# Kernel optimization log

Hardware: AMD Instinct MI355X
Metric: run time of the kernel (lower is better)

The kernel has to match this reference:

```python
import jax, jax.numpy as jnp
import numpy as np

DIM = 768
NUM_HEADS = 12
HEAD_DIM = DIM // NUM_HEADS
SCALE = HEAD_DIM ** -0.5
B, N = 16, 640  # N = 8*8 + 24*24


def setup_inputs() -> dict:
    key = jax.random.key(0)
    ks = jax.random.split(key, 4)
    x = jax.random.normal(ks[0], (B, N, DIM), dtype=jnp.float32)
    # weights stored input-major: y = x @ W + b (equiv. to torch Linear with W = weight.T)
    qkv_w = jax.random.normal(ks[1], (DIM, 3 * DIM), dtype=jnp.float32) * (DIM ** -0.5)
    qkv_b = jnp.zeros((3 * DIM,), dtype=jnp.float32)
    proj_w = jax.random.normal(ks[2], (DIM, DIM), dtype=jnp.float32) * (DIM ** -0.5)
    proj_b = jnp.zeros((DIM,), dtype=jnp.float32)
    w = jnp.ones((2,), dtype=jnp.float32)
    return {"x": x, "qkv_w": qkv_w, "qkv_b": qkv_b, "proj_w": proj_w,
            "proj_b": proj_b, "w": w, "t_h": 8, "t_w": 8, "s_h": 24, "s_w": 24}


def reference(x, qkv_w, qkv_b, proj_w, proj_b, w, t_h, t_w, s_h, s_w):
    b, n, c = x.shape
    qkv = (x @ qkv_w + qkv_b).reshape(b, n, 3, NUM_HEADS, HEAD_DIM)
    qkv = jnp.transpose(qkv, (2, 0, 3, 1, 4))  # [3, B, H, N, D]
    q, k, v = qkv[0], qkv[1], qkv[2]
    attn = jnp.einsum('bhnd,bhmd->bhnm', q, k) * SCALE  # [B,H,N,N]
    attn0 = jax.nn.softmax(attn, axis=-1)
    attn1 = jnp.square(jax.nn.relu(attn))
    ws = jax.nn.softmax(w)  # exp(w_i)/sum(exp(w)) blend weights
    attn = attn0 * ws[0] + attn1 * ws[1]
    out = jnp.einsum('bhnm,bhmd->bhnd', attn, v)  # [B,H,N,D]
    out = jnp.transpose(out, (0, 2, 1, 3)).reshape(b, n, c)
    return out @ proj_w + proj_b
```

## Files before the change

### kernel.cpp

```cpp
#include <hip/hip_runtime.h>
#include <hip/hip_bf16.h>

typedef __attribute__((ext_vector_type(8))) short short8;
typedef __attribute__((ext_vector_type(4))) float floatx4;
typedef __hip_bfloat16 bf16;

#define DIM 768
#define NH 12
#define HD 64
#define BB 16
#define NN 640
#define BH (BB*NH)
#define MROWS (BB*NN)
#define QKVN (3*DIM)
#define QSCALE 0.18033688011113205f
#define LN2SQ 0.4804530139182014f

#define CVT_BLK (MROWS*DIM/4/256)
#define TRQ_BLK ((QKVN/32)*(DIM/32))
#define TRP_BLK ((DIM/32)*(DIM/32))

__device__ __forceinline__ floatx4 mfma16(short8 a, short8 b, floatx4 c) {
    return __builtin_amdgcn_mfma_f32_16x16x32_bf16(a, b, c, 0, 0, 0);
}

__device__ __forceinline__ void async_ld16(const bf16* g, bf16* l) {
    __builtin_amdgcn_global_load_lds(
        (const __attribute__((address_space(1))) void*)g,
        (__attribute__((address_space(3))) void*)l, 16, 0, 0);
}

__device__ __forceinline__ unsigned pack_trunc(float a, float b) {
    return __builtin_amdgcn_perm(__float_as_uint(b), __float_as_uint(a), 0x07060302u);
}

__device__ __forceinline__ unsigned pack_rne(float a, float b) {
    unsigned sa = (unsigned)__bfloat16_as_ushort(__float2bfloat16(a));
    unsigned sb = (unsigned)__bfloat16_as_ushort(__float2bfloat16(b));
    return sa | (sb << 16);
}

__device__ __forceinline__ float fexp2(float x) {
#if __has_builtin(__builtin_amdgcn_exp2f)
    return __builtin_amdgcn_exp2f(x);
#else
    return exp2f(x);
#endif
}

__global__ void prep_all(const float* __restrict__ x,
                         const float* __restrict__ qkv_w,
                         const float* __restrict__ proj_w,
                         bf16* __restrict__ xb,
                         bf16* __restrict__ qwT,
                         bf16* __restrict__ pwT)
{
    __shared__ float tile[32][33];
    const int id = blockIdx.x;
    const int t = threadIdx.x;

    if (id < CVT_BLK) {
        int i = id * 256 + t;
        float4 v = ((const float4*)x)[i];
        *(uint2*)(xb + (size_t)i * 4) =
            make_uint2(pack_rne(v.x, v.y), pack_rne(v.z, v.w));
        return;
    }

    const float* src; bf16* dst; int C, bx, by;
    if (id < CVT_BLK + TRQ_BLK) {
        int j = id - CVT_BLK;
        bx = j % (QKVN/32); by = j / (QKVN/32);
        src = qkv_w; dst = qwT; C = QKVN;
    } else {
        int j = id - CVT_BLK - TRQ_BLK;
        bx = j % (DIM/32); by = j / (DIM/32);
        src = proj_w; dst = pwT; C = DIM;
    }
    const int R = DIM;
    const int tx = t & 31, ty = t >> 5;
    for (int j = 0; j < 4; ++j)
        tile[ty + j*8][tx] = src[(size_t)(by*32 + ty + j*8) * C + bx*32 + tx];
    __syncthreads();
    for (int j = 0; j < 4; ++j)
        dst[(size_t)(bx*32 + ty + j*8) * R + by*32 + tx] = __float2bfloat16(tile[tx][ty + j*8]);
}

template<int MODE>
__global__ __launch_bounds__(256) void gemm_bt(
    const bf16* __restrict__ A, const bf16* __restrict__ B, const float* __restrict__ bias,
    int M, int N, int K,
    bf16* __restrict__ outb, bf16* __restrict__ vTo, float* __restrict__ outf)
{
    __shared__ __align__(16) bf16 As[2][128*64];
    __shared__ __align__(16) bf16 Bs[2][128*64];

    const int t = threadIdx.x;
    const int lane = t & 63, wave = t >> 6;
    const int l15 = lane & 15, quad = lane >> 4;
    const int wm = (wave >> 1) * 64, wn = (wave & 1) * 64;

    constexpr int GX  = (MODE == 0) ? (QKVN/128) : (DIM/128);
    constexpr int NWG = GX * (MROWS/128);
    constexpr int CHUNK = NWG / 8;
    int lin = blockIdx.y * GX + blockIdx.x;
    lin = (lin & 7) * CHUNK + (lin >> 3);
    const int m0 = (lin / GX) * 128, n0 = (lin % GX) * 128;

    floatx4 acc[4][4];
    floatx4 zero = {0.f, 0.f, 0.f, 0.f};
    for (int i = 0; i < 4; ++i)
        for (int j = 0; j < 4; ++j)
            acc[i][j] = zero;

    const int trow = t >> 3;
    const int gc = ((t & 7) ^ (trow & 7)) << 3;
    const bf16* aA = A + (size_t)(m0 + trow) * K + gc;
    const bf16* aB = B + (size_t)(n0 + trow) * K + gc;
    const int lb = wave * 512;

    for (int s = 0; s < 4; ++s) {
        async_ld16(aA + (size_t)s*32*K, &As[0][s*2048 + lb]);
        async_ld16(aB + (size_t)s*32*K, &Bs[0][s*2048 + lb]);
    }

    const int sw = l15 & 7;
    const int nit = K >> 6;
    for (int kt = 0; kt < nit; ++kt) {
        const int cur = kt & 1;
        __syncthreads();
        if (kt + 1 < nit) {
            const bf16* pA = aA + (size_t)(kt+1)*64;
            const bf16* pB = aB + (size_t)(kt+1)*64;
            for (int s = 0; s < 4; ++s) {
                async_ld16(pA + (size_t)s*32*K, &As[cur^1][s*2048 + lb]);
                async_ld16(pB + (size_t)s*32*K, &Bs[cur^1][s*2048 + lb]);
            }
        }
        short8 af0[4], af1[4], bf0[4], bf1[4];
        for (int fm = 0; fm < 4; ++fm) {
            int base = (wm + fm*16 + l15) * 64 + ((quad ^ sw) << 3);
            af0[fm] = *(const short8*)(&As[cur][base]);
            af1[fm] = *(const short8*)(&As[cur][base ^ 32]);
        }
        for (int fn = 0; fn < 4; ++fn) {
            int base = (wn + fn*16 + l15) * 64 + ((quad ^ sw) << 3);
            bf0[fn] = *(const short8*)(&Bs[cur][base]);
            bf1[fn] = *(const short8*)(&Bs[cur][base ^ 32]);
        }
        for (int fm = 0; fm < 4; ++fm)
            for (int fn = 0; fn < 4; ++fn) {
                acc[fm][fn] = mfma16(bf0[fn], af0[fm], acc[fm][fn]);
                acc[fm][fn] = mfma16(bf1[fn], af1[fm], acc[fm][fn]);
            }
    }

    if (MODE == 0 && n0 >= 2*DIM) {
        bf16* S = &As[0][0] + wave * 2048;
        unsigned short* Su = (unsigned short*)S;
        const int bh   = (m0 / NN) * NH + ((n0 + wn) >> 6) - 24;
        const int tokb = (m0 % NN) + wm;
        const int dl = lane >> 2, cc = (lane & 3) * 16;
        for (int fn = 0; fn < 4; ++fn) {
            int nb = n0 + wn + fn*16 + quad*4;
            float4 bv = *(const float4*)(bias + nb);
            float bvr[4] = {bv.x, bv.y, bv.z, bv.w};
            for (int fm = 0; fm < 4; ++fm) {
#pragma unroll
                for (int r = 0; r < 4; ++r) {
                    float v = acc[fm][fn][r] + bvr[r];
                    Su[(quad*4 + r)*72 + fm*16 + l15] =
                        (unsigned short)(__float_as_uint(v) >> 16);
                }
            }
            uint4 r0 = *(const uint4*)(S + dl*72 + cc);
            uint4 r1 = *(const uint4*)(S + dl*72 + cc + 8);
            bf16* dst = vTo + ((size_t)bh * HD + fn*16 + dl) * NN + tokb + cc;
            *(uint4*)dst = r0;
            *(uint4*)(dst + 8) = r1;
        }
        return;
    }

    for (int fm = 0; fm < 4; ++fm) {
        int m = m0 + wm + fm*16 + l15;
        if (MODE == 0) {
            bf16* row = outb + (size_t)m * N;
            for (int fn = 0; fn < 4; ++fn) {
                int n = n0 + wn + fn*16 + quad*4;
                float4 bv = *(const float4*)(bias + n);
                float v0 = acc[fm][fn][0] + bv.x;
                float v1 = acc[fm][fn][1] + bv.y;
                float v2 = acc[fm][fn][2] + bv.z;
                float v3 = acc[fm][fn][3] + bv.w;
                if (n < DIM) {
                    v0 *= QSCALE; v1 *= QSCALE; v2 *= QSCALE; v3 *= QSCALE;
                }
                *(uint2*)(row + n) = make_uint2(pack_rne(v0, v1), pack_rne(v2, v3));
            }
        } else {
            float* row = outf + (size_t)m * N;
            for (int fn = 0; fn < 4; ++fn) {
                int n = n0 + wn + fn*16 + quad*4;
                float4 bv = *(const float4*)(bias + n);
                float4 v;
                v.x = acc[fm][fn][0] + bv.x;
                v.y = acc[fm][fn][1] + bv.y;
                v.z = acc[fm][fn][2] + bv.z;
                v.w = acc[fm][fn][3] + bv.w;
                *(float4*)(row + n) = v;
            }
        }
    }
}

__global__ __launch_bounds__(256) void attn_kernel(
    const bf16* __restrict__ qkv, const bf16* __restrict__ vT,
    const float* __restrict__ w2, bf16* __restrict__ ao)
{
    int lin = blockIdx.y * BH + blockIdx.x;
    int j = lin >> 3;
    const int bh = (lin & 7) + 8 * (j / 10);
    const int qt = j % 10;
    const int b = bh / NH, h = bh - b * NH;
    const int t = threadIdx.x;
    const int wave = t >> 6, lane = t & 63;
    const int l15 = lane & 15, quad = lane >> 4;
    const int qrow0 = qt * 64 + wave * 16;

    float w0 = w2[0], w1 = w2[1];
    float wmx = fmaxf(w0, w1);
    float e0 = __expf(w0 - wmx), e1 = __expf(w1 - wmx);
    float ws0 = e0 / (e0 + e1);
    float ws1 = (1.0f - ws0) * LN2SQ;

    __shared__ __align__(16) bf16 Kb[2][64*64];
    __shared__ __align__(16) bf16 Vb[2][64*64];
    __shared__ __align__(16) bf16 Ps[4][16*72];
    __shared__ __align__(16) bf16 Pr[4][16*72];

    const bf16* kb = qkv + (size_t)(b*NN)*QKVN + DIM + h*HD;
    const bf16* vb = vT + (size_t)bh * HD * NN;

    const bf16* qr = qkv + (size_t)(b*NN + qrow0 + l15) * QKVN + h*HD;
    short8 aq0 = *(const short8*)(qr + quad*8);
    short8 aq1 = *(const short8*)(qr + 32 + quad*8);

    const int srow = t >> 3;
    const int gc   = ((lane & 7) ^ (lane >> 3)) << 3;
    const bf16* kst = kb + (size_t)srow * QKVN + gc;
    const bf16* vst = vb + (size_t)srow * NN + gc;
    const int lb0 = (wave * 64) * 8;
    const int lb1 = (256 + wave * 64) * 8;

    async_ld16(kst,                     &Kb[0][lb0]);
    async_ld16(kst + (size_t)32 * QKVN, &Kb[0][lb1]);
    async_ld16(vst,                     &Vb[0][lb0]);
    async_ld16(vst + (size_t)32 * NN,   &Vb[0][lb1]);

    floatx4 zero = {0.f, 0.f, 0.f, 0.f};
    floatx4 accS[4], accR[4];
    for (int i = 0; i < 4; ++i) { accS[i] = zero; accR[i] = zero; }
    float lsum = 0.f;

    const int sw = l15 & 7;
    const int fbase = l15 * 64 + ((quad ^ sw) << 3);

    unsigned* PsW = (unsigned*)&Ps[wave][0];
    unsigned* PrW = (unsigned*)&Pr[wave][0];
    const int wb = l15*36 + quad*2;
    const bf16* PsR = &Ps[wave][l15*72 + quad*8];
    const bf16* PrR = &Pr[wave][l15*72 + quad*8];

#pragma unroll 2
    for (int kt = 0; kt < 10; ++kt) {
        const int cur = kt & 1;
        __syncthreads();
        if (kt + 1 < 10) {
            kst += (size_t)64 * QKVN;
            vst += 64;
            async_ld16(kst,                     &Kb[cur^1][lb0]);
            async_ld16(kst + (size_t)32 * QKVN, &Kb[cur^1][lb1]);
            async_ld16(vst,                     &Vb[cur^1][lb0]);
            async_ld16(vst + (size_t)32 * NN,   &Vb[cur^1][lb1]);
        }

        const bf16* Kc = &Kb[cur][0];
        const bf16* Vc = &Vb[cur][0];

        floatx4 s[4];
        for (int I = 0; I < 4; ++I) {
            short8 aklo = *(const short8*)(Kc + fbase + I*1024);
            short8 akhi = *(const short8*)(Kc + ((fbase + I*1024) ^ 32));
            s[I] = zero;
            s[I] = mfma16(aklo, aq0, s[I]);
            s[I] = mfma16(akhi, aq1, s[I]);
        }

        short8 bvlo[4], bvhi[4];
        for (int dt = 0; dt < 4; ++dt) {
            bvlo[dt] = *(const short8*)(Vc + fbase + dt*1024);
            bvhi[dt] = *(const short8*)(Vc + ((fbase + dt*1024) ^ 32));
        }

        for (int I = 0; I < 4; ++I) {
            float ex[4], rq[4];
            for (int r = 0; r < 4; ++r) {
                ex[r] = fexp2(s[I][r]);
                float m = fmaxf(s[I][r], 0.f);
                rq[r] = m * m;
                lsum += ex[r];
            }
            *(uint2*)(PsW + wb + I*8) = make_uint2(pack_trunc(ex[0],ex[1]), pack_trunc(ex[2],ex[3]));
            *(uint2*)(PrW + wb + I*8) = make_uint2(pack_trunc(rq[0],rq[1]), pack_trunc(rq[2],rq[3]));
        }

        short8 paSlo = *(const short8*)PsR;
        short8 paShi = *(const short8*)(PsR + 32);
        short8 paRlo = *(const short8*)PrR;
        short8 paRhi = *(const short8*)(PrR + 32);

        for (int dt = 0; dt < 4; ++dt) {
            accS[dt] = mfma16(paSlo, bvlo[dt], accS[dt]);
            accS[dt] = mfma16(paShi, bvhi[dt], accS[dt]);
            accR[dt] = mfma16(paRlo, bvlo[dt], accR[dt]);
            accR[dt] = mfma16(paRhi, bvhi[dt], accR[dt]);
        }
    }

    lsum += __shfl_xor(lsum, 16);
    lsum += __shfl_xor(lsum, 32);
    float invq[4];
    for (int r = 0; r < 4; ++r)
        invq[r] = 1.0f / __shfl(lsum, quad*4 + r);

    for (int dt = 0; dt < 4; ++dt) {
        for (int r = 0; r < 4; ++r) {
            float v = ws0 * accS[dt][r] * invq[r] + ws1 * accR[dt][r];
            int tok = qrow0 + quad*4 + r;
            ao[((size_t)(b * NN + tok)) * DIM + h * HD + dt*16 + l15] = __float2bfloat16(v);
        }
    }
}


extern "C" void kernel_launch(void* const* d_in, const int* in_sizes, int n_in,
                              void* d_out, int out_size, void* d_ws, size_t ws_size,
                              hipStream_t stream) {
    const float* x      = (const float*)d_in[0];
    const float* qkv_w  = (const float*)d_in[1];
    const float* qkv_b  = (const float*)d_in[2];
    const float* proj_w = (const float*)d_in[3];
    const float* proj_b = (const float*)d_in[4];
    const float* w2     = (const float*)d_in[5];
    float* out = (float*)d_out;

    bf16* xb   = (bf16*)d_ws;
    bf16* qwT  = xb   + (size_t)MROWS * DIM;
    bf16* pwT  = qwT  + (size_t)QKVN * DIM;
    bf16* qkvb = pwT  + (size_t)DIM * DIM;
    bf16* vT   = qkvb + (size_t)MROWS * QKVN;
    bf16* ao   = xb;

    prep_all<<<CVT_BLK + TRQ_BLK + TRP_BLK, 256, 0, stream>>>(
        x, qkv_w, proj_w, xb, qwT, pwT);

    gemm_bt<0><<<dim3(QKVN / 128, MROWS / 128), 256, 0, stream>>>(
        xb, qwT, qkv_b, MROWS, QKVN, DIM, qkvb, vT, nullptr);

    attn_kernel<<<dim3(BH, NN / 64), 256, 0, stream>>>(qkvb, vT, w2, ao);

    gemm_bt<1><<<dim3(DIM / 128, MROWS / 128), 256, 0, stream>>>(
        ao, pwT, proj_b, MROWS, DIM, DIM, nullptr, nullptr, out);
}
```

Before: 217.7 us.

## Add 256x256-tile 8-wave QKV GEMM with phased async staging

Replaces the 128x128 QKV projection GEMM with a dedicated kernel that uses 256x256 output tiles, 512 threads, and a four-phase-per-buffer schedule. Global-to-LDS async loads are interleaved with MFMA phases, using setprio and explicit waitcnt/barriers. The aim is to raise arithmetic intensity and hide load latency. It uses 128KB of LDS per block, and the grid becomes 9x40 = 360 blocks, which may leave CUs unevenly loaded. The V-transpose epilogue is reworked for the new wave layout.

Result: slower. 227.4 us (+4.4%).

```diff
diff --git a/kernel.cpp b/kernel.cpp
--- a/kernel.cpp
+++ b/kernel.cpp
@@ -84,6 +84,179 @@
     __syncthreads();
     for (int j = 0; j < 4; ++j)
         dst[(size_t)(bx*32 + ty + j*8) * R + by*32 + tx] = __float2bfloat16(tile[tx][ty + j*8]);
+}
+
+__global__ __launch_bounds__(512, 2) void gemm_qkv256(
+    const bf16* __restrict__ A, const bf16* __restrict__ B, const float* __restrict__ bias,
+    bf16* __restrict__ outb, bf16* __restrict__ vTo)
+{
+    constexpr int K = DIM;
+    constexpr int N = QKVN;
+    __shared__ __align__(16) bf16 As[2][2][128*64];
+    __shared__ __align__(16) bf16 Bs[2][2][128*64];
+
+    const int t = threadIdx.x;
+    const int lane = t & 63, wave = t >> 6;
+    const int l15 = lane & 15, quad = lane >> 4;
+    const int wm = wave >> 2;
+    const int wn = wave & 3;
+    const int hB = wn >> 1;
+    const int m0 = blockIdx.y * 256, n0 = blockIdx.x * 256;
+
+    floatx4 acc[8][4];
+    floatx4 zero = {0.f, 0.f, 0.f, 0.f};
+#pragma unroll
+    for (int i = 0; i < 8; ++i)
+#pragma unroll
+        for (int j = 0; j < 4; ++j)
+            acc[i][j] = zero;
+
+    const int trow = t >> 3;
+    const int gc = ((t & 7) ^ (trow & 7)) << 3;
+    const bf16* Ag = A + (size_t)(m0 + trow) * K + gc;
+    const bf16* Bg = B + (size_t)(n0 + trow) * K + gc;
+    const int tb = t * 8;
+
+#define STG_A(buf,h,s,tcol) async_ld16(Ag + (size_t)((h)*128+(s)*64)*K + (tcol), &As[buf][h][(s)*4096 + tb])
+#define STG_B(buf,h,s,tcol) async_ld16(Bg + (size_t)((h)*128+(s)*64)*K + (tcol), &Bs[buf][h][(s)*4096 + tb])
+
+    const int swq = (quad ^ (l15 & 7)) << 3;
+    const int aoff = l15 * 64 + swq;
+    const int boff = (wn & 1) * 4096 + l15 * 64 + swq;
+
+    short8 bfr[4][2];
+
+#define RD_B(buf) do { \
+    _Pragma("unroll") \
+    for (int fn = 0; fn < 4; ++fn) { \
+        const int _ob = boff + fn*1024; \
+        bfr[fn][0] = *(const short8*)&Bs[buf][hB][_ob]; \
+        bfr[fn][1] = *(const short8*)&Bs[buf][hB][_ob ^ 32]; \
+    } } while (0)
+
+#define PHASE(buf, q, RB, STAGES, WAITS) do { \
+    const int _o = aoff + (2*(q))*1024; \
+    short8 a00 = *(const short8*)&As[buf][wm][_o]; \
+    short8 a01 = *(const short8*)&As[buf][wm][_o ^ 32]; \
+    short8 a10 = *(const short8*)&As[buf][wm][_o + 1024]; \
+    short8 a11 = *(const short8*)&As[buf][wm][(_o + 1024) ^ 32]; \
+    RB; \
+    STAGES; \
+    __builtin_amdgcn_s_barrier(); \
+    asm volatile("s_waitcnt lgkmcnt(0)" ::: "memory"); \
+    __builtin_amdgcn_sched_barrier(0); \
+    __builtin_amdgcn_s_setprio(1); \
+    _Pragma("unroll") \
+    for (int fn = 0; fn < 4; ++fn) { \
+        acc[2*(q)][fn]   = mfma16(bfr[fn][0], a00, acc[2*(q)][fn]); \
+        acc[2*(q)+1][fn] = mfma16(bfr[fn][0], a10, acc[2*(q)+1][fn]); \
+    } \
+    _Pragma("unroll") \
+    for (int fn = 0; fn < 4; ++fn) { \
+        acc[2*(q)][fn]   = mfma16(bfr[fn][1], a01, acc[2*(q)][fn]); \
+        acc[2*(q)+1][fn] = mfma16(bfr[fn][1], a11, acc[2*(q)+1][fn]); \
+    } \
+    __builtin_amdgcn_s_setprio(0); \
+    WAITS; \
+    __builtin_amdgcn_s_barrier(); \
+} while (0)
+
+    STG_B(0,0,0,0); STG_B(0,0,1,0); STG_B(0,1,0,0); STG_B(0,1,1,0);
+    STG_A(0,0,0,0); STG_A(0,1,0,0); STG_A(0,0,1,0); STG_A(0,1,1,0);
+    STG_B(1,0,0,64); STG_B(1,0,1,64); STG_B(1,1,0,64); STG_B(1,1,1,64);
+    STG_A(1,0,0,64); STG_A(1,1,0,64);
+    asm volatile("s_waitcnt vmcnt(6)" ::: "memory");
+    __builtin_amdgcn_s_barrier();
+
+    for (int it = 0; it < 6; ++it) {
+        const int kb = it * 128;
+        const bool more = (it < 5);
+        PHASE(0, 0, RD_B(0),
+              { STG_A(1,0,1,kb+64); STG_A(1,1,1,kb+64); },
+              (void)0);
+        PHASE(0, 1, (void)0,
+              { if (more) { STG_B(0,0,0,kb+128); STG_B(0,0,1,kb+128); } },
+              (void)0);
+        PHASE(0, 2, (void)0,
+              { if (more) { STG_B(0,1,0,kb+128); STG_B(0,1,1,kb+128); } },
+              (void)0);
+        PHASE(0, 3, (void)0,
+              { if (more) { STG_A(0,0,0,kb+128); STG_A(0,1,0,kb+128); } },
+              { if (more) { asm volatile("s_waitcnt vmcnt(6)" ::: "memory"); }
+                else      { asm volatile("s_waitcnt vmcnt(0)" ::: "memory"); } });
+        PHASE(1, 0, RD_B(1),
+              { if (more) { STG_A(0,0,1,kb+128); STG_A(0,1,1,kb+128); } },
+              (void)0);
+        PHASE(1, 1, (void)0,
+              { if (more) { STG_B(1,0,0,kb+192); STG_B(1,0,1,kb+192); } },
+              (void)0);
+        PHASE(1, 2, (void)0,
+              { if (more) { STG_B(1,1,0,kb+192); STG_B(1,1,1,kb+192); } },
+              (void)0);
+        PHASE(1, 3, (void)0,
+              { if (more) { STG_A(1,0,0,kb+192); STG_A(1,1,0,kb+192); } },
+              { if (more) { asm volatile("s_waitcnt vmcnt(6)" ::: "memory"); } });
+    }
+#undef PHASE
+#undef RD_B
+#undef STG_A
+#undef STG_B
+
+    const int mb = m0 + wm * 128;
+    const int nb = n0 + wn * 64;
+
+    if (n0 >= 2*DIM) {
+        bf16* S = &As[0][0][0] + wave * 2048;
+        unsigned short* Su = (unsigned short*)S;
+        const int head = (nb - 2*DIM) >> 6;
+        const int gm = mb;
+        const int bh = (gm / NN) * NH + head;
+        const int tokb = gm % NN;
+        const int dl = lane >> 2, cc = (lane & 3) * 16;
+#pragma unroll
+        for (int fmh = 0; fmh < 2; ++fmh) {
+#pragma unroll
+            for (int fn = 0; fn < 4; ++fn) {
+                int nq = nb + fn*16 + quad*4;
+                float4 bv = *(const float4*)(bias + nq);
+                float bvr[4] = {bv.x, bv.y, bv.z, bv.w};
+#pragma unroll
+                for (int fi = 0; fi < 4; ++fi) {
+#pragma unroll
+                    for (int r = 0; r < 4; ++r) {
+                        float v = acc[fmh*4 + fi][fn][r] + bvr[r];
+                        Su[(quad*4 + r)*72 + fi*16 + l15] =
+                            (unsigned short)(__float_as_uint(v) >> 16);
+                    }
+                }
+                uint4 r0 = *(const uint4*)(S + dl*72 + cc);
+                uint4 r1 = *(const uint4*)(S + dl*72 + cc + 8);
+                int d = fn*16 + dl;
+                bf16* dst = vTo + ((size_t)bh * HD + d) * NN + tokb + fmh*64 + cc;
+                *(uint4*)dst = r0;
+                *(uint4*)(dst + 8) = r1;
+            }
+        }
+        return;
+    }
+
+    const bool isq = (n0 < DIM);
+#pragma unroll
+    for (int fm = 0; fm < 8; ++fm) {
+        int m = mb + fm*16 + l15;
+        bf16* row = outb + (size_t)m * N;
+#pragma unroll
+        for (int fn = 0; fn < 4; ++fn) {
+            int n = nb + fn*16 + quad*4;
+            float4 bv = *(const float4*)(bias + n);
+            float v0 = acc[fm][fn][0] + bv.x;
+            float v1 = acc[fm][fn][1] + bv.y;
+            float v2 = acc[fm][fn][2] + bv.z;
+            float v3 = acc[fm][fn][3] + bv.w;
+            if (isq) { v0 *= QSCALE; v1 *= QSCALE; v2 *= QSCALE; v3 *= QSCALE; }
+            *(uint2*)(row + n) = make_uint2(pack_rne(v0, v1), pack_rne(v2, v3));
+        }
+    }
 }
 
 template<int MODE>
@@ -365,8 +538,8 @@
     prep_all<<<CVT_BLK + TRQ_BLK + TRP_BLK, 256, 0, stream>>>(
         x, qkv_w, proj_w, xb, qwT, pwT);
 
-    gemm_bt<0><<<dim3(QKVN / 128, MROWS / 128), 256, 0, stream>>>(
-        xb, qwT, qkv_b, MROWS, QKVN, DIM, qkvb, vT, nullptr);
+    gemm_qkv256<<<dim3(QKVN / 256, MROWS / 256), 512, 0, stream>>>(
+        xb, qwT, qkv_b, qkvb, vT);
 
     attn_kernel<<<dim3(BH, NN / 64), 256, 0, stream>>>(qkvb, vT, w2, ao);
 
```

## Use 256x128 tiles with 8 waves and ping-pong scheduled GEMM pipeline

Applied to the files above, without the earlier changes.

Replaces the 128x128, 4-wave GEMM with a 256x128-tile, 8-wave kernel with compile-time shapes. The K loop is software-pipelined: each step stages two 64-wide K slices, explicit vmcnt/lgkmcnt waits and barriers interleave global loads with MFMA halves, and s_setprio raises priority during MFMA. The aim is better tile reuse and overlap of memory traffic with matrix math in both the QKV and output-projection GEMMs. In exchange it relies on hand-tuned wait counts and uses more shared memory, and the larger tiles give fewer workgroups.

Result: slower. 225.3 us (+3.5%).

```diff
diff --git a/kernel.cpp b/kernel.cpp
--- a/kernel.cpp
+++ b/kernel.cpp
@@ -87,84 +87,133 @@
 }
 
 template<int MODE>
-__global__ __launch_bounds__(256) void gemm_bt(
+__global__ __launch_bounds__(512, 2) void gemm256(
     const bf16* __restrict__ A, const bf16* __restrict__ B, const float* __restrict__ bias,
-    int M, int N, int K,
     bf16* __restrict__ outb, bf16* __restrict__ vTo, float* __restrict__ outf)
 {
-    __shared__ __align__(16) bf16 As[2][128*64];
+    constexpr int K = DIM;
+    constexpr int N = (MODE == 0) ? QKVN : DIM;
+    constexpr int GX = N / 128;
+    constexpr int NWG = GX * (MROWS / 256);
+    constexpr int CHUNK = NWG / 8;
+
+    __shared__ __align__(16) bf16 As[2][256*64];
     __shared__ __align__(16) bf16 Bs[2][128*64];
 
     const int t = threadIdx.x;
     const int lane = t & 63, wave = t >> 6;
     const int l15 = lane & 15, quad = lane >> 4;
-    const int wm = (wave >> 1) * 64, wn = (wave & 1) * 64;
-
-    constexpr int GX  = (MODE == 0) ? (QKVN/128) : (DIM/128);
-    constexpr int NWG = GX * (MROWS/128);
-    constexpr int CHUNK = NWG / 8;
-    int lin = blockIdx.y * GX + blockIdx.x;
+    const int wm = wave >> 1;
+    const int wn = wave & 1;
+
+    int lin = blockIdx.x;
     lin = (lin & 7) * CHUNK + (lin >> 3);
-    const int m0 = (lin / GX) * 128, n0 = (lin % GX) * 128;
+    const int m0 = (lin / GX) * 256, n0 = (lin % GX) * 128;
 
     floatx4 acc[4][4];
     floatx4 zero = {0.f, 0.f, 0.f, 0.f};
+#pragma unroll
     for (int i = 0; i < 4; ++i)
+#pragma unroll
         for (int j = 0; j < 4; ++j)
             acc[i][j] = zero;
 
     const int trow = t >> 3;
     const int gc = ((t & 7) ^ (trow & 7)) << 3;
-    const bf16* aA = A + (size_t)(m0 + trow) * K + gc;
-    const bf16* aB = B + (size_t)(n0 + trow) * K + gc;
-    const int lb = wave * 512;
-
-    for (int s = 0; s < 4; ++s) {
-        async_ld16(aA + (size_t)s*32*K, &As[0][s*2048 + lb]);
-        async_ld16(aB + (size_t)s*32*K, &Bs[0][s*2048 + lb]);
-    }
-
-    const int sw = l15 & 7;
-    const int nit = K >> 6;
-    for (int kt = 0; kt < nit; ++kt) {
-        const int cur = kt & 1;
-        __syncthreads();
-        if (kt + 1 < nit) {
-            const bf16* pA = aA + (size_t)(kt+1)*64;
-            const bf16* pB = aB + (size_t)(kt+1)*64;
-            for (int s = 0; s < 4; ++s) {
-                async_ld16(pA + (size_t)s*32*K, &As[cur^1][s*2048 + lb]);
-                async_ld16(pB + (size_t)s*32*K, &Bs[cur^1][s*2048 + lb]);
-            }
-        }
-        short8 af0[4], af1[4], bf0[4], bf1[4];
-        for (int fm = 0; fm < 4; ++fm) {
-            int base = (wm + fm*16 + l15) * 64 + ((quad ^ sw) << 3);
-            af0[fm] = *(const short8*)(&As[cur][base]);
-            af1[fm] = *(const short8*)(&As[cur][base ^ 32]);
-        }
-        for (int fn = 0; fn < 4; ++fn) {
-            int base = (wn + fn*16 + l15) * 64 + ((quad ^ sw) << 3);
-            bf0[fn] = *(const short8*)(&Bs[cur][base]);
-            bf1[fn] = *(const short8*)(&Bs[cur][base ^ 32]);
-        }
-        for (int fm = 0; fm < 4; ++fm)
-            for (int fn = 0; fn < 4; ++fn) {
-                acc[fm][fn] = mfma16(bf0[fn], af0[fm], acc[fm][fn]);
-                acc[fm][fn] = mfma16(bf1[fn], af1[fm], acc[fm][fn]);
-            }
-    }
+    const bf16* Ag = A + (size_t)(m0 + trow) * K + gc;
+    const bf16* Bg = B + (size_t)(n0 + trow) * K + gc;
+    const int tb = t * 8;
+
+#define STG_A(buf,s,tcol) async_ld16(Ag + (size_t)(s)*64*K + (tcol), &As[buf][(s)*4096 + tb])
+#define STG_B(buf,s,tcol) async_ld16(Bg + (size_t)(s)*64*K + (tcol), &Bs[buf][(s)*4096 + tb])
+
+    const int sw8 = (quad ^ (l15 & 7)) << 3;
+    const int aoff = (wm*64 + l15) * 64 + sw8;
+    const int boff = (wn*64 + l15) * 64 + sw8;
+
+    short8 afr[4][2], bfr[4][2];
+
+#define RD_FRAGS(buf) do { \
+    _Pragma("unroll") \
+    for (int f = 0; f < 4; ++f) { \
+        afr[f][0] = *(const short8*)&As[buf][aoff + f*1024]; \
+        afr[f][1] = *(const short8*)&As[buf][(aoff + f*1024) ^ 32]; \
+        bfr[f][0] = *(const short8*)&Bs[buf][boff + f*1024]; \
+        bfr[f][1] = *(const short8*)&Bs[buf][(boff + f*1024) ^ 32]; \
+    } } while (0)
+
+#define MFMA_HALF(q) do { \
+    __builtin_amdgcn_s_setprio(1); \
+    _Pragma("unroll") \
+    for (int fn = 0; fn < 4; ++fn) { \
+        acc[2*(q)][fn]   = mfma16(bfr[fn][0], afr[2*(q)][0],   acc[2*(q)][fn]); \
+        acc[2*(q)+1][fn] = mfma16(bfr[fn][0], afr[2*(q)+1][0], acc[2*(q)+1][fn]); \
+    } \
+    _Pragma("unroll") \
+    for (int fn = 0; fn < 4; ++fn) { \
+        acc[2*(q)][fn]   = mfma16(bfr[fn][1], afr[2*(q)][1],   acc[2*(q)][fn]); \
+        acc[2*(q)+1][fn] = mfma16(bfr[fn][1], afr[2*(q)+1][1], acc[2*(q)+1][fn]); \
+    } \
+    __builtin_amdgcn_s_setprio(0); \
+} while (0)
+
+    STG_A(0,0,0); STG_A(0,1,0); STG_A(0,2,0); STG_A(0,3,0);
+    STG_B(0,0,0); STG_B(0,1,0);
+    STG_A(1,0,64); STG_A(1,1,64); STG_A(1,2,64); STG_A(1,3,64);
+    STG_B(1,0,64); STG_B(1,1,64);
+    asm volatile("s_waitcnt vmcnt(6)" ::: "memory");
+    __builtin_amdgcn_s_barrier();
+
+    for (int it = 0; it < 6; ++it) {
+        const int kb = it * 128;
+        const bool more = (it < 5);
+        RD_FRAGS(0);
+        __builtin_amdgcn_s_barrier();
+        asm volatile("s_waitcnt lgkmcnt(0)" ::: "memory");
+        __builtin_amdgcn_sched_barrier(0);
+        MFMA_HALF(0);
+        __builtin_amdgcn_s_barrier();
+        if (more) { STG_A(0,0,kb+128); STG_A(0,1,kb+128); STG_A(0,2,kb+128); STG_A(0,3,kb+128); }
+        MFMA_HALF(1);
+        __builtin_amdgcn_sched_barrier(0);
+        if (more) { asm volatile("s_waitcnt vmcnt(4)" ::: "memory"); }
+        else      { asm volatile("s_waitcnt vmcnt(0)" ::: "memory"); }
+        __builtin_amdgcn_s_barrier();
+        RD_FRAGS(1);
+        if (more) { STG_B(0,0,kb+128); STG_B(0,1,kb+128); }
+        __builtin_amdgcn_s_barrier();
+        asm volatile("s_waitcnt lgkmcnt(0)" ::: "memory");
+        __builtin_amdgcn_sched_barrier(0);
+        MFMA_HALF(0);
+        __builtin_amdgcn_s_barrier();
+        if (more) { STG_A(1,0,kb+192); STG_A(1,1,kb+192); STG_A(1,2,kb+192); STG_A(1,3,kb+192);
+                    STG_B(1,0,kb+192); STG_B(1,1,kb+192); }
+        MFMA_HALF(1);
+        __builtin_amdgcn_sched_barrier(0);
+        if (more) { asm volatile("s_waitcnt vmcnt(6)" ::: "memory"); }
+        __builtin_amdgcn_s_barrier();
+    }
+#undef RD_FRAGS
+#undef MFMA_HALF
+#undef STG_A
+#undef STG_B
+
+    const int mb = m0 + wm * 64;
+    const int nb = n0 + wn * 64;
 
     if (MODE == 0 && n0 >= 2*DIM) {
         bf16* S = &As[0][0] + wave * 2048;
         unsigned short* Su = (unsigned short*)S;
-        const int bh   = (m0 / NN) * NH + ((n0 + wn) >> 6) - 24;
-        const int tokb = (m0 % NN) + wm;
+        const int head = ((nb - 2*DIM) >> 6);
+        const int bh = (mb / NN) * NH + head;
+        const int tokb = mb % NN;
         const int dl = lane >> 2, cc = (lane & 3) * 16;
+#pragma unroll
         for (int fn = 0; fn < 4; ++fn) {
-            int nb = n0 + wn + fn*16 + quad*4;
-            float4 bv = *(const float4*)(bias + nb);
+            int nq = nb + fn*16 + quad*4;
+            float4 bv = *(const float4*)(bias + nq);
             float bvr[4] = {bv.x, bv.y, bv.z, bv.w};
+#pragma unroll
             for (int fm = 0; fm < 4; ++fm) {
 #pragma unroll
                 for (int r = 0; r < 4; ++r) {
@@ -175,33 +224,40 @@
             }
             uint4 r0 = *(const uint4*)(S + dl*72 + cc);
             uint4 r1 = *(const uint4*)(S + dl*72 + cc + 8);
-            bf16* dst = vTo + ((size_t)bh * HD + fn*16 + dl) * NN + tokb + cc;
+            int d = fn*16 + dl;
+            bf16* dst = vTo + ((size_t)bh * HD + d) * NN + tokb + cc;
             *(uint4*)dst = r0;
             *(uint4*)(dst + 8) = r1;
         }
         return;
     }
 
-    for (int fm = 0; fm < 4; ++fm) {
-        int m = m0 + wm + fm*16 + l15;
-        if (MODE == 0) {
+    if (MODE == 0) {
+        const bool isq = (n0 < DIM);
+#pragma unroll
+        for (int fm = 0; fm < 4; ++fm) {
+            int m = mb + fm*16 + l15;
             bf16* row = outb + (size_t)m * N;
+#pragma unroll
             for (int fn = 0; fn < 4; ++fn) {
-                int n = n0 + wn + fn*16 + quad*4;
+                int n = nb + fn*16 + quad*4;
                 float4 bv = *(const float4*)(bias + n);
                 float v0 = acc[fm][fn][0] + bv.x;
                 float v1 = acc[fm][fn][1] + bv.y;
                 float v2 = acc[fm][fn][2] + bv.z;
                 float v3 = acc[fm][fn][3] + bv.w;
-                if (n < DIM) {
-                    v0 *= QSCALE; v1 *= QSCALE; v2 *= QSCALE; v3 *= QSCALE;
-                }
+                if (isq) { v0 *= QSCALE; v1 *= QSCALE; v2 *= QSCALE; v3 *= QSCALE; }
                 *(uint2*)(row + n) = make_uint2(pack_rne(v0, v1), pack_rne(v2, v3));
             }
-        } else {
+        }
+    } else {
+#pragma unroll
+        for (int fm = 0; fm < 4; ++fm) {
+            int m = mb + fm*16 + l15;
             float* row = outf + (size_t)m * N;
+#pragma unroll
             for (int fn = 0; fn < 4; ++fn) {
-                int n = n0 + wn + fn*16 + quad*4;
+                int n = nb + fn*16 + quad*4;
                 float4 bv = *(const float4*)(bias + n);
                 float4 v;
                 v.x = acc[fm][fn][0] + bv.x;
@@ -365,11 +421,11 @@
     prep_all<<<CVT_BLK + TRQ_BLK + TRP_BLK, 256, 0, stream>>>(
         x, qkv_w, proj_w, xb, qwT, pwT);
 
-    gemm_bt<0><<<dim3(QKVN / 128, MROWS / 128), 256, 0, stream>>>(
-        xb, qwT, qkv_b, MROWS, QKVN, DIM, qkvb, vT, nullptr);
+    gemm256<0><<<dim3((QKVN/128) * (MROWS/256)), 512, 0, stream>>>(
+        xb, qwT, qkv_b, qkvb, vT, nullptr);
 
     attn_kernel<<<dim3(BH, NN / 64), 256, 0, stream>>>(qkvb, vT, w2, ao);
 
-    gemm_bt<1><<<dim3(DIM / 128, MROWS / 128), 256, 0, stream>>>(
-        ao, pwT, proj_b, MROWS, DIM, DIM, nullptr, nullptr, out);
-}
+    gemm256<1><<<dim3((DIM/128) * (MROWS/256)), 512, 0, stream>>>(
+        ao, pwT, proj_b, nullptr, nullptr, out);
+}
```

## Add dedicated 256x192-tile QKV GEMM with 8-wave ping-pong pipeline

Applied to the files above, without the earlier changes.

Replaces the generic 128x128 QKV GEMM with a dedicated kernel that uses 256x192 tiles, 512 threads, a double-buffered async global-to-LDS load schedule with explicit waitcnt/barrier placement, MFMA priority boosting and an XCD-aware block remap. The larger tile raises arithmetic intensity and cuts the number of workgroups, and the staged interleaving aims to overlap loads with MFMA work. In exchange it uses more LDS and registers per block, and the hand-written waitcnt sequencing is fragile. The old generic kernel keeps only the projection path.

Measured after the change: 216.6 us. About the same (-0.5%).

```diff
diff --git a/kernel.cpp b/kernel.cpp
--- a/kernel.cpp
+++ b/kernel.cpp
@@ -84,6 +84,195 @@
     __syncthreads();
     for (int j = 0; j < 4; ++j)
         dst[(size_t)(bx*32 + ty + j*8) * R + by*32 + tx] = __float2bfloat16(tile[tx][ty + j*8]);
+}
+
+__global__ __launch_bounds__(512, 2) void gemm_qkv(
+    const bf16* __restrict__ A, const bf16* __restrict__ B, const float* __restrict__ bias,
+    bf16* __restrict__ outb, bf16* __restrict__ vTo)
+{
+    constexpr int K = DIM;
+    constexpr int N = QKVN;
+    constexpr int GX = N / 192;
+    constexpr int NWG = GX * (MROWS / 256);
+    constexpr int CHUNK = NWG / 8;
+
+    __shared__ __align__(16) bf16 As[2][256*64];
+    __shared__ __align__(16) bf16 Bs[2][192*64];
+
+    const int t = threadIdx.x;
+    const int lane = t & 63, wave = t >> 6;
+    const int l15 = lane & 15, quad = lane >> 4;
+    const int wm = wave >> 1;
+    const int wn = wave & 1;
+
+    int lin = blockIdx.x;
+    lin = (lin & 7) * CHUNK + (lin >> 3);
+    const int m0 = (lin / GX) * 256, n0 = (lin % GX) * 192;
+
+    floatx4 acc[4][6];
+    floatx4 zero = {0.f, 0.f, 0.f, 0.f};
+#pragma unroll
+    for (int i = 0; i < 4; ++i)
+#pragma unroll
+        for (int j = 0; j < 6; ++j)
+            acc[i][j] = zero;
+
+    const int trow = t >> 3;
+    const int gc = ((t & 7) ^ (trow & 7)) << 3;
+    const bf16* Ag = A + (size_t)(m0 + trow) * K + gc;
+    const bf16* Bg = B + (size_t)(n0 + trow) * K + gc;
+    const int tb = t * 8;
+
+#define STG_A(buf,s,tcol) async_ld16(Ag + (size_t)(s)*64*K + (tcol), &As[buf][(s)*4096 + tb])
+#define STG_B(buf,s,tcol) async_ld16(Bg + (size_t)(s)*64*K + (tcol), &Bs[buf][(s)*4096 + tb])
+
+    const int sw8 = (quad ^ (l15 & 7)) << 3;
+    const int aoff = (wm*64 + l15) * 64 + sw8;
+    const int boff = (wn*96 + l15) * 64 + sw8;
+
+    short8 afr[4][2], bfr[2][2];
+
+#define RD_A(buf) do { \
+    _Pragma("unroll") \
+    for (int f = 0; f < 4; ++f) { \
+        afr[f][0] = *(const short8*)&As[buf][aoff + f*1024]; \
+        afr[f][1] = *(const short8*)&As[buf][(aoff + f*1024) ^ 32]; \
+    } } while (0)
+
+#define RD_B2(buf, fp) do { \
+    bfr[0][0] = *(const short8*)&Bs[buf][boff + (2*(fp))*1024]; \
+    bfr[0][1] = *(const short8*)&Bs[buf][(boff + (2*(fp))*1024) ^ 32]; \
+    bfr[1][0] = *(const short8*)&Bs[buf][boff + (2*(fp)+1)*1024]; \
+    bfr[1][1] = *(const short8*)&Bs[buf][(boff + (2*(fp)+1)*1024) ^ 32]; \
+    } while (0)
+
+#define MFMA16(fp) do { \
+    __builtin_amdgcn_s_setprio(1); \
+    _Pragma("unroll") \
+    for (int fm = 0; fm < 4; ++fm) { \
+        acc[fm][2*(fp)]   = mfma16(bfr[0][0], afr[fm][0], acc[fm][2*(fp)]); \
+        acc[fm][2*(fp)+1] = mfma16(bfr[1][0], afr[fm][0], acc[fm][2*(fp)+1]); \
+    } \
+    _Pragma("unroll") \
+    for (int fm = 0; fm < 4; ++fm) { \
+        acc[fm][2*(fp)]   = mfma16(bfr[0][1], afr[fm][1], acc[fm][2*(fp)]); \
+        acc[fm][2*(fp)+1] = mfma16(bfr[1][1], afr[fm][1], acc[fm][2*(fp)+1]); \
+    } \
+    __builtin_amdgcn_s_setprio(0); \
+} while (0)
+
+#define BAR_LG0() do { \
+    __builtin_amdgcn_s_barrier(); \
+    asm volatile("s_waitcnt lgkmcnt(0)" ::: "memory"); \
+    __builtin_amdgcn_sched_barrier(0); \
+} while (0)
+
+    STG_A(0,0,0); STG_A(0,1,0); STG_A(0,2,0); STG_A(0,3,0);
+    STG_B(0,0,0); STG_B(0,1,0); STG_B(0,2,0);
+    STG_A(1,0,64); STG_A(1,1,64); STG_A(1,2,64); STG_A(1,3,64);
+    asm volatile("s_waitcnt vmcnt(4)" ::: "memory");
+    __builtin_amdgcn_s_barrier();
+
+    for (int it = 0; it < 6; ++it) {
+        const int kb = it * 128;
+        const bool more = (it < 5);
+        RD_A(0); RD_B2(0, 0);
+        STG_B(1,0,kb+64); STG_B(1,1,kb+64); STG_B(1,2,kb+64);
+        asm volatile("s_waitcnt lgkmcnt(8)" ::: "memory");
+        BAR_LG0();
+        MFMA16(0);
+        __builtin_amdgcn_sched_barrier(0);
+        __builtin_amdgcn_s_barrier();
+        RD_B2(0, 1);
+        if (more) { STG_A(0,0,kb+128); STG_A(0,1,kb+128); STG_A(0,2,kb+128); STG_A(0,3,kb+128); }
+        BAR_LG0();
+        MFMA16(1);
+        __builtin_amdgcn_sched_barrier(0);
+        __builtin_amdgcn_s_barrier();
+        RD_B2(0, 2);
+        BAR_LG0();
+        MFMA16(2);
+        __builtin_amdgcn_sched_barrier(0);
+        if (more) { asm volatile("s_waitcnt vmcnt(4)" ::: "memory"); }
+        else      { asm volatile("s_waitcnt vmcnt(0)" ::: "memory"); }
+        __builtin_amdgcn_s_barrier();
+        RD_A(1); RD_B2(1, 0);
+        if (more) { STG_B(0,0,kb+128); STG_B(0,1,kb+128); STG_B(0,2,kb+128); }
+        asm volatile("s_waitcnt lgkmcnt(8)" ::: "memory");
+        BAR_LG0();
+        MFMA16(0);
+        __builtin_amdgcn_sched_barrier(0);
+        __builtin_amdgcn_s_barrier();
+        RD_B2(1, 1);
+        if (more) { STG_A(1,0,kb+192); STG_A(1,1,kb+192); STG_A(1,2,kb+192); STG_A(1,3,kb+192); }
+        BAR_LG0();
+        MFMA16(1);
+        __builtin_amdgcn_sched_barrier(0);
+        __builtin_amdgcn_s_barrier();
+        RD_B2(1, 2);
+        BAR_LG0();
+        MFMA16(2);
+        __builtin_amdgcn_sched_barrier(0);
+        if (more) { asm volatile("s_waitcnt vmcnt(4)" ::: "memory"); }
+        __builtin_amdgcn_s_barrier();
+    }
+#undef RD_A
+#undef RD_B2
+#undef MFMA16
+#undef BAR_LG0
+#undef STG_A
+#undef STG_B
+
+    const int mb = m0 + wm * 64;
+    const int nb = n0 + wn * 96;
+
+    if (n0 >= 2*DIM) {
+        bf16* S = &As[0][0] + wave * 2048;
+        unsigned short* Su = (unsigned short*)S;
+        const int batch = mb / NN;
+        const int tokb = mb % NN;
+        const int dl = lane >> 2, cc = (lane & 3) * 16;
+#pragma unroll
+        for (int fn = 0; fn < 6; ++fn) {
+            int cb = nb + fn*16;
+            int bh = batch * NH + ((cb - 2*DIM) >> 6);
+            int dbase = cb & 63;
+            float4 bv = *(const float4*)(bias + cb + quad*4);
+            float bvr[4] = {bv.x, bv.y, bv.z, bv.w};
+#pragma unroll
+            for (int fm = 0; fm < 4; ++fm) {
+#pragma unroll
+                for (int r = 0; r < 4; ++r) {
+                    float v = acc[fm][fn][r] + bvr[r];
+                    Su[(quad*4 + r)*72 + fm*16 + l15] =
+                        (unsigned short)(__float_as_uint(v) >> 16);
+                }
+            }
+            uint4 r0 = *(const uint4*)(S + dl*72 + cc);
+            uint4 r1 = *(const uint4*)(S + dl*72 + cc + 8);
+            bf16* dst = vTo + ((size_t)bh * HD + dbase + dl) * NN + tokb + cc;
+            *(uint4*)dst = r0;
+            *(uint4*)(dst + 8) = r1;
+        }
+        return;
+    }
+
+#pragma unroll
+    for (int fm = 0; fm < 4; ++fm) {
+        int m = mb + fm*16 + l15;
+        bf16* row = outb + (size_t)m * N;
+#pragma unroll
+        for (int fn = 0; fn < 6; ++fn) {
+            int n = nb + fn*16 + quad*4;
+            float4 bv = *(const float4*)(bias + n);
+            float v0 = acc[fm][fn][0] + bv.x;
+            float v1 = acc[fm][fn][1] + bv.y;
+            float v2 = acc[fm][fn][2] + bv.z;
+            float v3 = acc[fm][fn][3] + bv.w;
+            if (n < DIM) { v0 *= QSCALE; v1 *= QSCALE; v2 *= QSCALE; v3 *= QSCALE; }
+            *(uint2*)(row + n) = make_uint2(pack_rne(v0, v1), pack_rne(v2, v3));
+        }
+    }
 }
 
 template<int MODE>
@@ -155,61 +344,18 @@
             }
     }
 
-    if (MODE == 0 && n0 >= 2*DIM) {
-        bf16* S = &As[0][0] + wave * 2048;
-        unsigned short* Su = (unsigned short*)S;
-        const int bh   = (m0 / NN) * NH + ((n0 + wn) >> 6) - 24;
-        const int tokb = (m0 % NN) + wm;
-        const int dl = lane >> 2, cc = (lane & 3) * 16;
-        for (int fn = 0; fn < 4; ++fn) {
-            int nb = n0 + wn + fn*16 + quad*4;
-            float4 bv = *(const float4*)(bias + nb);
-            float bvr[4] = {bv.x, bv.y, bv.z, bv.w};
-            for (int fm = 0; fm < 4; ++fm) {
-#pragma unroll
-                for (int r = 0; r < 4; ++r) {
-                    float v = acc[fm][fn][r] + bvr[r];
-                    Su[(quad*4 + r)*72 + fm*16 + l15] =
-                        (unsigned short)(__float_as_uint(v) >> 16);
-                }
-            }
-            uint4 r0 = *(const uint4*)(S + dl*72 + cc);
-            uint4 r1 = *(const uint4*)(S + dl*72 + cc + 8);
-            bf16* dst = vTo + ((size_t)bh * HD + fn*16 + dl) * NN + tokb + cc;
-            *(uint4*)dst = r0;
-            *(uint4*)(dst + 8) = r1;
-        }
-        return;
-    }
-
     for (int fm = 0; fm < 4; ++fm) {
         int m = m0 + wm + fm*16 + l15;
-        if (MODE == 0) {
-            bf16* row = outb + (size_t)m * N;
-            for (int fn = 0; fn < 4; ++fn) {
-                int n = n0 + wn + fn*16 + quad*4;
-                float4 bv = *(const float4*)(bias + n);
-                float v0 = acc[fm][fn][0] + bv.x;
-                float v1 = acc[fm][fn][1] + bv.y;
-                float v2 = acc[fm][fn][2] + bv.z;
-                float v3 = acc[fm][fn][3] + bv.w;
-                if (n < DIM) {
-                    v0 *= QSCALE; v1 *= QSCALE; v2 *= QSCALE; v3 *= QSCALE;
-                }
-                *(uint2*)(row + n) = make_uint2(pack_rne(v0, v1), pack_rne(v2, v3));
-            }
-        } else {
-            float* row = outf + (size_t)m * N;
-            for (int fn = 0; fn < 4; ++fn) {
-                int n = n0 + wn + fn*16 + quad*4;
-                float4 bv = *(const float4*)(bias + n);
-                float4 v;
-                v.x = acc[fm][fn][0] + bv.x;
-                v.y = acc[fm][fn][1] + bv.y;
-                v.z = acc[fm][fn][2] + bv.z;
-                v.w = acc[fm][fn][3] + bv.w;
-                *(float4*)(row + n) = v;
-            }
+        float* row = outf + (size_t)m * N;
+        for (int fn = 0; fn < 4; ++fn) {
+            int n = n0 + wn + fn*16 + quad*4;
+            float4 bv = *(const float4*)(bias + n);
+            float4 v;
+            v.x = acc[fm][fn][0] + bv.x;
+            v.y = acc[fm][fn][1] + bv.y;
+            v.z = acc[fm][fn][2] + bv.z;
+            v.w = acc[fm][fn][3] + bv.w;
+            *(float4*)(row + n) = v;
         }
     }
 }
@@ -365,8 +511,8 @@
     prep_all<<<CVT_BLK + TRQ_BLK + TRP_BLK, 256, 0, stream>>>(
         x, qkv_w, proj_w, xb, qwT, pwT);
 
-    gemm_bt<0><<<dim3(QKVN / 128, MROWS / 128), 256, 0, stream>>>(
-        xb, qwT, qkv_b, MROWS, QKVN, DIM, qkvb, vT, nullptr);
+    gemm_qkv<<<dim3((QKVN/192) * (MROWS/256)), 512, 0, stream>>>(
+        xb, qwT, qkv_b, qkvb, vT);
 
     attn_kernel<<<dim3(BH, NN / 64), 256, 0, stream>>>(qkvb, vT, w2, ao);
 
```
